# Kernel optimization log

Hardware: AMD Instinct MI355X
Metric: run time of the kernel (lower is better)

The kernel has to match this reference:

```python
import jax, jax.numpy as jnp
import numpy as np

NEG_INF = -1000000.0  # matches the original's -1e6 masking constant


def setup_inputs() -> dict:
    key = jax.random.key(0)
    ks = jax.random.split(key, 7)
    B, S, A, Q, D = 32, 2048, 1024, 1024, 1024  # batch, src len, attend_dim, query_dim, att_dim
    return {
        "input": jax.random.normal(ks[0], (B, 1, Q), dtype=jnp.float32),
        "context": jax.random.normal(ks[1], (B, S, A), dtype=jnp.float32),
        "W_pre": jax.random.normal(ks[2], (D, A), dtype=jnp.float32) * 0.02,
        "b_pre": jax.random.normal(ks[3], (D,), dtype=jnp.float32) * 0.02,
        "W_q": jax.random.normal(ks[4], (D, Q), dtype=jnp.float32) * 0.02,
        "v": jax.random.normal(ks[5], (D,), dtype=jnp.float32) * 0.02,
        "mask": jax.random.randint(ks[6], (B, 1, S), 0, 2, dtype=jnp.int32),
    }


def reference(input, context, W_pre, b_pre, W_q, v, mask):
    # precompute = linear_pre(context): [B, S, D]
    precompute = jnp.einsum("bsa,da->bsd", context, W_pre) + b_pre
    # targetT = linear_q(input): [B, 1, D]; repeat over S via broadcast
    targetT = jnp.einsum("bqc,dc->bqd", input, W_q)
    tmp = jnp.tanh(precompute + targetT)                 # [B, S, D]
    energy = jnp.einsum("bsd,d->bs", tmp, v)             # linear_v -> [B, S]
    # mask: positions where mask == 0 get -1e6 (energy*(1-m) + m*(-1e6), m = (mask==0))
    masked_out = (mask[:, 0, :] == 0)
    energy = jnp.where(masked_out, NEG_INF, energy)
    score = jax.nn.softmax(energy, axis=1)               # softmax over S
    score_m = score[:, None, :]                          # [B, 1, S]
    weightedContext = jnp.einsum("bqs,bsa->bqa", score_m, context)  # [B, 1, A]
    return weightedContext, score_m, precompute
```

## Files before the change

kernel.cpp:

```cpp
#include <hip/hip_runtime.h>

#define NEG_INF_VAL -1000000.0f

typedef short s16x8 __attribute__((ext_vector_type(8)));
typedef float f32x4 __attribute__((ext_vector_type(4)));

__device__ __forceinline__ unsigned int bf16_rne(float f) {
  unsigned int u = __float_as_uint(f);
  return (u + 0x7fffu + ((u >> 16) & 1u)) >> 16;
}
__device__ __forceinline__ unsigned int pack_bf2(float a, float b) {
  return bf16_rne(a) | (bf16_rne(b) << 16);
}

__device__ __forceinline__ float fast_tanh(float x) {
  float xc = fminf(fmaxf(x, -15.f), 15.f);
  float t = __expf(2.f * xc);
  return __fdividef(t - 1.f, t + 1.f);
}

__global__ __launch_bounds__(256) void convert_bf16_kernel(
    const float* __restrict__ src, unsigned short* __restrict__ dst, long n) {
  long i = ((long)blockIdx.x * blockDim.x + threadIdx.x) * 8;
  long stride = (long)gridDim.x * blockDim.x * 8;
  for (; i < n; i += stride) {
    float4 f0 = *(const float4*)(src + i);
    float4 f1 = *(const float4*)(src + i + 4);
    uint4 o;
    o.x = pack_bf2(f0.x, f0.y);
    o.y = pack_bf2(f0.z, f0.w);
    o.z = pack_bf2(f1.x, f1.y);
    o.w = pack_bf2(f1.z, f1.w);
    *(uint4*)(dst + i) = o;
  }
}

__global__ __launch_bounds__(256) void targetT_kernel(
    const float* __restrict__ input, const float* __restrict__ Wq,
    float* __restrict__ tT) {
  int d0 = blockIdx.x * 8;
  int t = threadIdx.x;
  int b = t >> 3, dl = t & 7;
  __shared__ float in_s[32][32];
  __shared__ float wq_s[8][32];
  float acc = 0.f;
  for (int q0 = 0; q0 < 1024; q0 += 32) {
    int r = t >> 3, c = (t & 7) * 4;
    *(float4*)&in_s[r][c] = *(const float4*)&input[r * 1024 + q0 + c];
    wq_s[t >> 5][t & 31] = Wq[(long)(d0 + (t >> 5)) * 1024 + q0 + (t & 31)];
    __syncthreads();
#pragma unroll
    for (int qq = 0; qq < 32; ++qq)
      acc += in_s[b][qq] * wq_s[dl][qq];
    __syncthreads();
  }
  tT[b * 1024 + d0 + dl] = acc;
}

__device__ __forceinline__ void load_lds16(const void* g, void* l) {
  __builtin_amdgcn_global_load_lds(
      (const __attribute__((address_space(1))) void*)g,
      (__attribute__((address_space(3))) void*)l, 16, 0, 0);
}

__global__ __launch_bounds__(256) void gemm_energy_kernel(
    const unsigned short* __restrict__ A,
    const unsigned short* __restrict__ B,
    const float* __restrict__ b_pre,
    const float* __restrict__ tT,
    const float* __restrict__ vvec,
    float* __restrict__ Cout,
    float* __restrict__ epart) {
  const int K = 1024;
  const int N = 1024;
  int lin = blockIdx.x;
  int w = (lin & 7) * 512 + (lin >> 3);
  int nt = w & 7;
  int mt = w >> 3;
  int m0 = mt * 128, n0 = nt * 128;
  int tid = threadIdx.x;
  int lane = tid & 63, wid = tid >> 6;
  int wr = wid >> 1, wc = wid & 1;

  __shared__ unsigned short sA[128][32];
  __shared__ unsigned short sB[128][32];

  f32x4 acc[4][4] = {};

  int srow = lane >> 2;
  int scol = ((lane & 3) ^ ((lane >> 3) & 3)) * 8;
  const unsigned short* Ag = A + (long)(m0 + wid * 32 + srow) * K + scol;
  const unsigned short* Bg = B + (long)(n0 + wid * 32 + srow) * K + scol;
  unsigned short* sA0 = &sA[wid * 32][0];
  unsigned short* sA1 = &sA[wid * 32 + 16][0];
  unsigned short* sB0 = &sB[wid * 32][0];
  unsigned short* sB1 = &sB[wid * 32 + 16][0];

  int r = lane & 15, g = lane >> 4;
  int slotA = (g ^ ((r >> 1) & 3)) * 8;

  for (int k0 = 0; k0 < K; k0 += 32) {
    load_lds16(Ag, sA0);
    load_lds16(Ag + 16 * K, sA1);
    load_lds16(Bg, sB0);
    load_lds16(Bg + 16 * K, sB1);
    Ag += 32; Bg += 32;
    asm volatile("s_waitcnt vmcnt(0)" ::: "memory");
    __syncthreads();
    s16x8 af[4], bfr[4];
#pragma unroll
    for (int i = 0; i < 4; ++i)
      af[i] = *(const s16x8*)&sA[wr * 64 + i * 16 + r][slotA];
#pragma unroll
    for (int j = 0; j < 4; ++j)
      bfr[j] = *(const s16x8*)&sB[wc * 64 + j * 16 + r][slotA];
#pragma unroll
    for (int i = 0; i < 4; ++i)
#pragma unroll
      for (int j = 0; j < 4; ++j)
        acc[i][j] = __builtin_amdgcn_mfma_f32_16x16x32_bf16(af[i], bfr[j], acc[i][j], 0, 0, 0);
    __syncthreads();
  }

  int b = m0 >> 11;
  float bp[4], tv[4], vv[4];
#pragma unroll
  for (int j = 0; j < 4; ++j) {
    int d = n0 + wc * 64 + j * 16 + r;
    bp[j] = b_pre[d];
    tv[j] = tT[b * 1024 + d];
    vv[j] = vvec[d];
  }
#pragma unroll
  for (int i = 0; i < 4; ++i) {
#pragma unroll
    for (int q = 0; q < 4; ++q) {
      int m = m0 + wr * 64 + i * 16 + g * 4 + q;
      float e = 0.f;
#pragma unroll
      for (int j = 0; j < 4; ++j) {
        float val = acc[i][j][q] + bp[j];
        Cout[(long)m * N + n0 + wc * 64 + j * 16 + r] = val;
        e += fast_tanh(val + tv[j]) * vv[j];
      }
      e += __shfl_xor(e, 1);
      e += __shfl_xor(e, 2);
      e += __shfl_xor(e, 4);
      e += __shfl_xor(e, 8);
      if (r == 0) epart[(long)m * 16 + nt * 2 + wc] = e;
    }
  }
}

__global__ __launch_bounds__(256) void softmax_kernel(
    const float* __restrict__ epart, const int* __restrict__ mask,
    float* __restrict__ score) {
  int b = blockIdx.x;
  int t = threadIdx.x;
  __shared__ float red[256];
  float ev[8];
  float mx = -3.4e38f;
#pragma unroll
  for (int ii = 0; ii < 8; ++ii) {
    int s = ii * 256 + t;
    long m = (long)b * 2048 + s;
    const float4* p = (const float4*)(epart + m * 16);
    float4 p0 = p[0], p1 = p[1], p2 = p[2], p3 = p[3];
    float e = p0.x + p0.y + p0.z + p0.w + p1.x + p1.y + p1.z + p1.w
            + p2.x + p2.y + p2.z + p2.w + p3.x + p3.y + p3.z + p3.w;
    if (mask[b * 2048 + s] == 0) e = NEG_INF_VAL;
    ev[ii] = e;
    mx = fmaxf(mx, e);
  }
  red[t] = mx; __syncthreads();
  for (int off = 128; off > 0; off >>= 1) {
    if (t < off) red[t] = fmaxf(red[t], red[t + off]);
    __syncthreads();
  }
  mx = red[0];
  __syncthreads();
  float sum = 0.f;
#pragma unroll
  for (int ii = 0; ii < 8; ++ii) { ev[ii] = __expf(ev[ii] - mx); sum += ev[ii]; }
  red[t] = sum; __syncthreads();
  for (int off = 128; off > 0; off >>= 1) {
    if (t < off) red[t] += red[t + off];
    __syncthreads();
  }
  float inv = 1.f / red[0];
#pragma unroll
  for (int ii = 0; ii < 8; ++ii)
    score[b * 2048 + ii * 256 + t] = ev[ii] * inv;
}

__global__ __launch_bounds__(256) void wc_partial_kernel(
    const unsigned short* __restrict__ ctx, const float* __restrict__ score,
    float* __restrict__ part) {
  int b = blockIdx.x, sc = blockIdx.y;
  int t = threadIdx.x;
  __shared__ float ssc[64];
  if (t < 64) ssc[t] = score[b * 2048 + sc * 64 + t];
  __syncthreads();
  float acc0 = 0.f, acc1 = 0.f, acc2 = 0.f, acc3 = 0.f;
  const unsigned short* cp = ctx + ((long)b * 2048 + sc * 64) * 1024 + t * 4;
  for (int s = 0; s < 64; ++s) {
    uint2 pk = *(const uint2*)cp;
    cp += 1024;
    float wgt = ssc[s];
    acc0 += wgt * __uint_as_float(pk.x << 16);
    acc1 += wgt * __uint_as_float(pk.x & 0xffff0000u);
    acc2 += wgt * __uint_as_float(pk.y << 16);
    acc3 += wgt * __uint_as_float(pk.y & 0xffff0000u);
  }
  float* pp = part + ((long)(b * 32 + sc)) * 1024 + t * 4;
  pp[0] = acc0; pp[1] = acc1; pp[2] = acc2; pp[3] = acc3;
}

__global__ __launch_bounds__(256) void wc_reduce_kernel(
    const float* __restrict__ part, float* __restrict__ wc) {
  int id = blockIdx.x * 256 + threadIdx.x;
  int b = id >> 10, a = id & 1023;
  float s = 0.f;
#pragma unroll
  for (int scn = 0; scn < 32; ++scn)
    s += part[((long)(b * 32 + scn)) * 1024 + a];
  wc[id] = s;
}

extern "C" void kernel_launch(void* const* d_in, const int* in_sizes, int n_in,
                              void* d_out, int out_size, void* d_ws, size_t ws_size,
                              hipStream_t stream) {
  const float* input   = (const float*)d_in[0];
  const float* context = (const float*)d_in[1];
  const float* W_pre   = (const float*)d_in[2];
  const float* b_pre   = (const float*)d_in[3];
  const float* W_q     = (const float*)d_in[4];
  const float* v       = (const float*)d_in[5];
  const int*   mask    = (const int*)d_in[6];

  float* out       = (float*)d_out;
  float* out_wc    = out;
  float* out_score = out + 32768;
  float* out_pre   = out + 98304;

  const size_t OFF_CTX   = 0;
  const size_t OFF_WPRE  = 134217728;
  const size_t OFF_TT    = 136314880;
  const size_t OFF_EPART = 136445952;
  const size_t OFF_WCP   = 140640256;
  const size_t WS_NEED   = 144834560;
  if (ws_size < WS_NEED) return;

  char* ws = (char*)d_ws;
  unsigned short* ctx_bf  = (unsigned short*)(ws + OFF_CTX);
  unsigned short* wpre_bf = (unsigned short*)(ws + OFF_WPRE);
  float* tT     = (float*)(ws + OFF_TT);
  float* epart  = (float*)(ws + OFF_EPART);
  float* wcpart = (float*)(ws + OFF_WCP);

  convert_bf16_kernel<<<2048, 256, 0, stream>>>(context, ctx_bf, 64LL * 1024 * 1024);
  convert_bf16_kernel<<<256, 256, 0, stream>>>(W_pre, wpre_bf, 1024LL * 1024);
  targetT_kernel<<<128, 256, 0, stream>>>(input, W_q, tT);
  gemm_energy_kernel<<<4096, 256, 0, stream>>>(ctx_bf, wpre_bf, b_pre, tT, v,
                                               out_pre, epart);
  softmax_kernel<<<32, 256, 0, stream>>>(epart, mask, out_score);
  dim3 g5(32, 32);
  wc_partial_kernel<<<g5, 256, 0, stream>>>(ctx_bf, out_score, wcpart);
  wc_reduce_kernel<<<128, 256, 0, stream>>>(wcpart, out_wc);
}
```

Measured before the change: 387.3 us.

## Enlarge GEMM tiles to 256x256 with double-buffered LDS prefetch

Rewrites the fused GEMM+energy kernel to use 256x256 output tiles with 512 threads and a K-step of 64. LDS is double-buffered so the next global-to-LDS load overlaps the MFMA work on the current buffer, with explicit waitcnt and barriers, and MFMA issue priority is raised via setprio. Larger tiles raise arithmetic intensity and cut global reloads of A and B. The cost is higher register pressure (8x4 accumulators) and 128KB of LDS per block, which limits occupancy.

```diff
diff --git a/kernel.cpp b/kernel.cpp
--- a/kernel.cpp
+++ b/kernel.cpp
@@ -63,7 +63,7 @@
       (__attribute__((address_space(3))) void*)l, 16, 0, 0);
 }
 
-__global__ __launch_bounds__(256) void gemm_energy_kernel(
+__global__ __launch_bounds__(512, 2) void gemm_energy_kernel(
     const unsigned short* __restrict__ A,
     const unsigned short* __restrict__ B,
     const float* __restrict__ b_pre,
@@ -72,82 +72,116 @@
     float* __restrict__ Cout,
     float* __restrict__ epart) {
   const int K = 1024;
-  const int N = 1024;
   int lin = blockIdx.x;
-  int w = (lin & 7) * 512 + (lin >> 3);
-  int nt = w & 7;
-  int mt = w >> 3;
-  int m0 = mt * 128, n0 = nt * 128;
+  int w = (lin & 7) * 128 + (lin >> 3);
+  int nt = w & 3;
+  int mt = w >> 2;
+  int m0 = mt * 256, n0 = nt * 256;
   int tid = threadIdx.x;
   int lane = tid & 63, wid = tid >> 6;
-  int wr = wid >> 1, wc = wid & 1;
-
-  __shared__ unsigned short sA[128][32];
-  __shared__ unsigned short sB[128][32];
-
-  f32x4 acc[4][4] = {};
-
-  int srow = lane >> 2;
-  int scol = ((lane & 3) ^ ((lane >> 3) & 3)) * 8;
-  const unsigned short* Ag = A + (long)(m0 + wid * 32 + srow) * K + scol;
-  const unsigned short* Bg = B + (long)(n0 + wid * 32 + srow) * K + scol;
-  unsigned short* sA0 = &sA[wid * 32][0];
-  unsigned short* sA1 = &sA[wid * 32 + 16][0];
-  unsigned short* sB0 = &sB[wid * 32][0];
-  unsigned short* sB1 = &sB[wid * 32 + 16][0];
-
+  int wr = wid >> 2, wc = wid & 3;
   int r = lane & 15, g = lane >> 4;
-  int slotA = (g ^ ((r >> 1) & 3)) * 8;
-
-  for (int k0 = 0; k0 < K; k0 += 32) {
-    load_lds16(Ag, sA0);
-    load_lds16(Ag + 16 * K, sA1);
-    load_lds16(Bg, sB0);
-    load_lds16(Bg + 16 * K, sB1);
-    Ag += 32; Bg += 32;
-    asm volatile("s_waitcnt vmcnt(0)" ::: "memory");
-    __syncthreads();
-    s16x8 af[4], bfr[4];
-#pragma unroll
-    for (int i = 0; i < 4; ++i)
-      af[i] = *(const s16x8*)&sA[wr * 64 + i * 16 + r][slotA];
-#pragma unroll
-    for (int j = 0; j < 4; ++j)
-      bfr[j] = *(const s16x8*)&sB[wc * 64 + j * 16 + r][slotA];
-#pragma unroll
-    for (int i = 0; i < 4; ++i)
+
+  __shared__ unsigned short sMem[2][2][256 * 64];
+
+  f32x4 acc[8][4] = {};
+
+  int rl = tid >> 3;
+  int swcol = ((tid & 7) ^ (rl & 7)) * 8;
+  const unsigned short* ap[4];
+  const unsigned short* bp[4];
+#pragma unroll
+  for (int j = 0; j < 4; ++j) {
+    ap[j] = A + (long)(m0 + j * 64 + rl) * K + swcol;
+    bp[j] = B + (long)(n0 + j * 64 + rl) * K + swcol;
+  }
+
+  auto stage = [&](int buf) {
+    char* la = (char*)&sMem[buf][0][0] + wid * 1024;
+    char* lb = (char*)&sMem[buf][1][0] + wid * 1024;
+#pragma unroll
+    for (int j = 0; j < 4; ++j) { load_lds16(ap[j], la + j * 8192); ap[j] += 64; }
+#pragma unroll
+    for (int j = 0; j < 4; ++j) { load_lds16(bp[j], lb + j * 8192); bp[j] += 64; }
+  };
+
+  auto compute = [&](int buf) {
+    const unsigned short* bA = &sMem[buf][0][0];
+    const unsigned short* bB = &sMem[buf][1][0];
+#pragma unroll
+    for (int kk = 0; kk < 2; ++kk) {
+      int slot = ((kk * 4 + g) ^ (r & 7)) * 8;
+      s16x8 af[8], bfv[4];
+#pragma unroll
+      for (int i = 0; i < 8; ++i)
+        af[i] = *(const s16x8*)(bA + (wr * 128 + i * 16 + r) * 64 + slot);
 #pragma unroll
       for (int j = 0; j < 4; ++j)
-        acc[i][j] = __builtin_amdgcn_mfma_f32_16x16x32_bf16(af[i], bfr[j], acc[i][j], 0, 0, 0);
-    __syncthreads();
-  }
+        bfv[j] = *(const s16x8*)(bB + (wc * 64 + j * 16 + r) * 64 + slot);
+      __builtin_amdgcn_s_setprio(1);
+#pragma unroll
+      for (int i = 0; i < 8; ++i)
+#pragma unroll
+        for (int j = 0; j < 4; ++j)
+          acc[i][j] = __builtin_amdgcn_mfma_f32_16x16x32_bf16(af[i], bfv[j], acc[i][j], 0, 0, 0);
+      __builtin_amdgcn_s_setprio(0);
+    }
+  };
+
+  stage(0);
+  stage(1);
+  asm volatile("s_waitcnt vmcnt(8)" ::: "memory");
+  __builtin_amdgcn_s_barrier();
+
+#pragma unroll 1
+  for (int it = 0; it < 7; ++it) {
+    compute(0);
+    asm volatile("s_waitcnt lgkmcnt(0)" ::: "memory");
+    __builtin_amdgcn_s_barrier();
+    stage(0);
+    asm volatile("s_waitcnt vmcnt(8)" ::: "memory");
+    __builtin_amdgcn_s_barrier();
+
+    compute(1);
+    asm volatile("s_waitcnt lgkmcnt(0)" ::: "memory");
+    __builtin_amdgcn_s_barrier();
+    stage(1);
+    asm volatile("s_waitcnt vmcnt(8)" ::: "memory");
+    __builtin_amdgcn_s_barrier();
+  }
+  compute(0);
+  asm volatile("s_waitcnt lgkmcnt(0)" ::: "memory");
+  __builtin_amdgcn_s_barrier();
+  asm volatile("s_waitcnt vmcnt(0)" ::: "memory");
+  __builtin_amdgcn_s_barrier();
+  compute(1);
 
   int b = m0 >> 11;
-  float bp[4], tv[4], vv[4];
+  float bias[4], tv[4], vv[4];
 #pragma unroll
   for (int j = 0; j < 4; ++j) {
     int d = n0 + wc * 64 + j * 16 + r;
-    bp[j] = b_pre[d];
+    bias[j] = b_pre[d];
     tv[j] = tT[b * 1024 + d];
     vv[j] = vvec[d];
   }
 #pragma unroll
-  for (int i = 0; i < 4; ++i) {
+  for (int i = 0; i < 8; ++i) {
 #pragma unroll
     for (int q = 0; q < 4; ++q) {
-      int m = m0 + wr * 64 + i * 16 + g * 4 + q;
+      int m = m0 + wr * 128 + i * 16 + g * 4 + q;
       float e = 0.f;
 #pragma unroll
       for (int j = 0; j < 4; ++j) {
-        float val = acc[i][j][q] + bp[j];
-        Cout[(long)m * N + n0 + wc * 64 + j * 16 + r] = val;
+        float val = acc[i][j][q] + bias[j];
+        Cout[(long)m * 1024 + n0 + wc * 64 + j * 16 + r] = val;
         e += fast_tanh(val + tv[j]) * vv[j];
       }
       e += __shfl_xor(e, 1);
       e += __shfl_xor(e, 2);
       e += __shfl_xor(e, 4);
       e += __shfl_xor(e, 8);
-      if (r == 0) epart[(long)m * 16 + nt * 2 + wc] = e;
+      if (r == 0) epart[(long)m * 16 + nt * 4 + wc] = e;
     }
   }
 }
@@ -261,7 +295,7 @@
   convert_bf16_kernel<<<2048, 256, 0, stream>>>(context, ctx_bf, 64LL * 1024 * 1024);
   convert_bf16_kernel<<<256, 256, 0, stream>>>(W_pre, wpre_bf, 1024LL * 1024);
   targetT_kernel<<<128, 256, 0, stream>>>(input, W_q, tT);
-  gemm_energy_kernel<<<4096, 256, 0, stream>>>(ctx_bf, wpre_bf, b_pre, tT, v,
+  gemm_energy_kernel<<<1024, 512, 0, stream>>>(ctx_bf, wpre_bf, b_pre, tT, v,
                                                out_pre, epart);
   softmax_kernel<<<32, 256, 0, stream>>>(epart, mask, out_score);
   dim3 g5(32, 32);
```

Result: faster. 363.5 us (-6.2%).
